# Kernel tuning notes

Measured on AMD Instinct MI355X. Metric: run time of the kernel, lower is better.

Reference implementation:

```python
import jax, jax.numpy as jnp
import numpy as np

B, N, IN_DIM, H, L = 8, 1024, 3, 256, 3
NUM_STEPS = 200
LN_EPS = 1e-5


def _cdist(a, b):
    # Euclidean pairwise distance, a:[B,n,d], b:[B,m,d] -> [B,n,m]
    d2 = (jnp.sum(a * a, -1)[:, :, None] + jnp.sum(b * b, -1)[:, None, :]
          - 2.0 * jnp.einsum('bik,bjk->bij', a, b))
    d2 = jnp.maximum(d2, 0.0)
    safe = jnp.sqrt(jnp.where(d2 > 0, d2, 1.0))
    return jnp.where(d2 > 0, safe, 0.0)


def _layernorm(x, g, b):
    mu = jnp.mean(x, -1, keepdims=True)
    var = jnp.mean(jnp.square(x - mu), -1, keepdims=True)
    return (x - mu) * jax.lax.rsqrt(var + LN_EPS) * g + b


def setup_inputs() -> dict:
    key = jax.random.key(0)
    ks = jax.random.split(key, 32)
    s = 0.02
    inp = {
        'x': jax.random.normal(ks[0], (B, N, IN_DIM), jnp.float32),
        't': jax.random.randint(ks[1], (B,), 0, NUM_STEPS),
        'mask': jnp.ones((B, N), bool),
        # top-level weights (stored [in,out])
        'w_time': jax.random.normal(ks[2], (1, H)) * s,
        'b_time': jnp.zeros((H,)),
        'w_in': jax.random.normal(ks[3], (IN_DIM + H, H)) * s,
        'b_in': jnp.zeros((H,)),
        'w_out': jax.random.normal(ks[4], (H, IN_DIM)) * s,
        'b_out': jnp.zeros((IN_DIM,)),
        # per-layer stacked params [L, ...]
        'qkv_w': jax.random.normal(ks[5], (L, H, 3 * H)) * s,
        'qkv_b': jnp.zeros((L, 3 * H)),
        'ao_w': jax.random.normal(ks[6], (L, H, H)) * s,
        'ao_b': jnp.zeros((L, H)),
        'fc1_w': jax.random.normal(ks[7], (L, H, 4 * H)) * s,
        'fc1_b': jax.random.normal(ks[8], (L, 4 * H)) * s,
        'fc2_w': jax.random.normal(ks[9], (L, 4 * H, H)) * s,
        'fc2_b': jax.random.normal(ks[10], (L, H)) * s,
        'ln1_g': jnp.ones((L, H)), 'ln1_b': jnp.zeros((L, H)),
        'ln2_g': jnp.ones((L, H)), 'ln2_b': jnp.zeros((L, H)),
    }
    return inp


def reference(x, t, mask, w_time, b_time, w_in, b_in, w_out, b_out,
              qkv_w, qkv_b, ao_w, ao_b, fc1_w, fc1_b, fc2_w, fc2_b,
              ln1_g, ln1_b, ln2_g, ln2_b):
    tf = t.astype(jnp.float32)[:, None] / float(NUM_STEPS)          # [B,1]
    t_embed = jax.nn.relu(tf @ w_time + b_time)                      # [B,H]
    t_embed = jnp.broadcast_to(t_embed[:, None, :], (B, N, H))
    h = jax.nn.relu(jnp.concatenate([x, t_embed], -1) @ w_in + b_in)  # [B,N,H]
    geo = _cdist(h[:, :, :3], h[:, :, :3])                           # [B,N,N]
    mask_f = mask.astype(h.dtype)
    scale = 1.0 / jnp.sqrt(jnp.float32(H))
    for l in range(L):
        qkv = (h @ qkv_w[l] + qkv_b[l]).reshape(B, N, 3, H)
        q, k, v = qkv[:, :, 0], qkv[:, :, 1], qkv[:, :, 2]
        dist = _cdist(geo, geo)                                      # cdist of the distance matrix itself
        scores = jnp.einsum('bik,bjk->bij', q, k) * scale * jnp.exp(-dist)
        scores = jnp.where(mask[:, None, :], scores, -jnp.inf)
        attn = jax.nn.softmax(scores, axis=-1)
        ao = (jnp.einsum('bij,bjk->bik', attn, v) @ ao_w[l] + ao_b[l]) * mask_f[:, :, None]
        xx = _layernorm(h + ao, ln1_g[l], ln1_b[l])
        f1 = jax.nn.relu((xx @ fc1_w[l] + fc1_b[l]) * mask_f[:, :, None])
        ffn = jax.nn.relu((f1 @ fc2_w[l] + fc2_b[l]) * mask_f[:, :, None])
        h = _layernorm(xx + ffn, ln2_g[l], ln2_b[l])
    return (h @ w_out + b_out) * mask_f[:, :, None]
```

## Files before the change

kernel.cpp:

```cpp
#include <hip/hip_runtime.h>
#include <math.h>

#define NB 8
#define NN 1024
#define NH 256
#define NL 3

typedef unsigned short u16;
typedef __bf16 bf16x8 __attribute__((ext_vector_type(8)));
typedef _Float16 f16x8 __attribute__((ext_vector_type(8)));
typedef float f32x4 __attribute__((ext_vector_type(4)));

constexpr int EPI_BIAS_RELU = 2, EPI_EDIST = 5, EPI_QKV = 6;

__device__ __forceinline__ unsigned bf16rne(float f) {
    unsigned u = __float_as_uint(f);
    return (u + 0x7fffu + ((u >> 16) & 1u)) >> 16;
}
__device__ __forceinline__ unsigned bfpair(float a, float b) {
    return bf16rne(a) | (bf16rne(b) << 16);
}
__device__ __forceinline__ float bf2f(u16 h) {
    unsigned u = ((unsigned)h) << 16;
    return __uint_as_float(u);
}

__device__ __forceinline__ float blockSum256(float v) {
    __shared__ float sm[4];
    #pragma unroll
    for (int o = 32; o; o >>= 1) v += __shfl_down(v, o, 64);
    int lane = threadIdx.x & 63, wid = threadIdx.x >> 6;
    if (lane == 0) sm[wid] = v;
    __syncthreads();
    if (threadIdx.x == 0) sm[0] = sm[0] + sm[1] + sm[2] + sm[3];
    __syncthreads();
    float r = sm[0];
    __syncthreads();
    return r;
}

template <int EPI, int DT, bool OBF, int SWZ, int MT>
__global__ __launch_bounds__(256) void gemm_mfma(
    const u16* __restrict__ A, int lda, long sA,
    const u16* __restrict__ Bt, int ldb, long sB,
    void* __restrict__ C, int ldc, long sC,
    int K,
    const float* __restrict__ bias, long sBias,
    u16* __restrict__ vtout)
{
    constexpr int MF = MT / 32;
    constexpr int ASZ = MT * 8;
    __shared__ uint4 sm4[ASZ + 1024];
    const int tid = threadIdx.x;

    int bx = blockIdx.x, by = blockIdx.y, bz = blockIdx.z;
    bool trans = false;
    if (SWZ == 2) {
        int gx = gridDim.x;
        int T = gx * gridDim.y;
        int lid = bx + gx * by;
        int nl = (lid & 7) * (T >> 3) + (lid >> 3);
        bx = nl % gx; by = nl / gx;
    } else if (SWZ == 3) {
        int lid = bx + gridDim.x * bz;
        bz = lid & 7;
        int idx = lid >> 3;
        int j = 0;
        while (idx >= 16 - 2 * j) { idx -= 16 - 2 * j; j++; }
        by = 2 * j + idx;
        bx = j;
        trans = (by >= 2 * bx + 2);
    }
    const int z = bz;
    const int row0 = by * MT, col0 = bx * 128;

    f32x4 acc[MF][4];
    #pragma unroll
    for (int m = 0; m < MF; m++)
        #pragma unroll
        for (int n = 0; n < 4; n++) acc[m][n] = (f32x4){0.f, 0.f, 0.f, 0.f};

    const int l = tid & 63, wid = tid >> 6;
    const int wr = wid >> 1, wc = wid & 1;
    const int lrow = l & 15, lgrp = l >> 4;

    for (int k0 = 0; k0 < K; k0 += 64) {
        if (MT == 128) {
            const int srow = tid >> 1, half = tid & 1, cb = half * 4, swz = srow & 7;
            const u16* Ap = A + (long)z * sA + (long)(row0 + srow) * lda + k0 + half * 32;
            uint4 a0 = *(const uint4*)(Ap + 0),  a1 = *(const uint4*)(Ap + 8);
            uint4 a2 = *(const uint4*)(Ap + 16), a3 = *(const uint4*)(Ap + 24);
            sm4[srow * 8 + ((cb + 0) ^ swz)] = a0;
            sm4[srow * 8 + ((cb + 1) ^ swz)] = a1;
            sm4[srow * 8 + ((cb + 2) ^ swz)] = a2;
            sm4[srow * 8 + ((cb + 3) ^ swz)] = a3;
        } else {
            const int arow = tid >> 2, aq = tid & 3, swz = arow & 7;
            const u16* Ap = A + (long)z * sA + (long)(row0 + arow) * lda + k0 + aq * 16;
            uint4 a0 = *(const uint4*)(Ap + 0), a1 = *(const uint4*)(Ap + 8);
            sm4[arow * 8 + ((aq * 2 + 0) ^ swz)] = a0;
            sm4[arow * 8 + ((aq * 2 + 1) ^ swz)] = a1;
        }
        {
            const int brow = tid >> 1, bq = tid & 1, cb = bq * 4, swz = brow & 7;
            const u16* Bp = Bt + (long)z * sB + (long)(col0 + brow) * ldb + k0 + bq * 32;
            uint4 b0 = *(const uint4*)(Bp + 0),  b1 = *(const uint4*)(Bp + 8);
            uint4 b2 = *(const uint4*)(Bp + 16), b3 = *(const uint4*)(Bp + 24);
            sm4[ASZ + brow * 8 + ((cb + 0) ^ swz)] = b0;
            sm4[ASZ + brow * 8 + ((cb + 1) ^ swz)] = b1;
            sm4[ASZ + brow * 8 + ((cb + 2) ^ swz)] = b2;
            sm4[ASZ + brow * 8 + ((cb + 3) ^ swz)] = b3;
        }
        __syncthreads();

        #pragma unroll
        for (int ks = 0; ks < 2; ks++) {
            int c = ks * 4 + lgrp;
            uint4 a[MF], b[4];
            #pragma unroll
            for (int m = 0; m < MF; m++) {
                int r = wr * (MT / 2) + m * 16 + lrow;
                a[m] = sm4[r * 8 + (c ^ (r & 7))];
            }
            #pragma unroll
            for (int n = 0; n < 4; n++) {
                int r = wc * 64 + n * 16 + lrow;
                b[n] = sm4[ASZ + r * 8 + (c ^ (r & 7))];
            }
            #pragma unroll
            for (int m = 0; m < MF; m++)
                #pragma unroll
                for (int n = 0; n < 4; n++) {
                    if (DT == 0)
                        acc[m][n] = __builtin_amdgcn_mfma_f32_16x16x32_bf16(
                            __builtin_bit_cast(bf16x8, a[m]), __builtin_bit_cast(bf16x8, b[n]), acc[m][n], 0, 0, 0);
                    else
                        acc[m][n] = __builtin_amdgcn_mfma_f32_16x16x32_f16(
                            __builtin_bit_cast(f16x8, a[m]), __builtin_bit_cast(f16x8, b[n]), acc[m][n], 0, 0, 0);
                }
        }
        __syncthreads();
    }

    u16* Ts = (u16*)sm4;
    #pragma unroll
    for (int m = 0; m < MF; m++) {
        #pragma unroll
        for (int n = 0; n < 4; n++) {
            int rbase = row0 + wr * (MT / 2) + m * 16 + lgrp * 4;
            int cc = col0 + wc * 64 + n * 16 + lrow;
            float bv = 0.f;
            if (EPI == EPI_QKV || EPI == EPI_BIAS_RELU)
                bv = bias[cc];
            float vals[4];
            #pragma unroll
            for (int reg = 0; reg < 4; reg++) {
                long r = rbase + reg;
                float v = acc[m][n][reg];
                if (EPI == EPI_QKV) v += bv;
                else if (EPI == EPI_BIAS_RELU) v = fmaxf(v + bv, 0.f);
                else if (EPI == EPI_EDIST) {
                    const float* rnb = bias + (long)z * sBias;
                    float d2 = fmaxf(rnb[r] + rnb[cc] - 2.f * v, 0.f);
                    v = (r == cc) ? 1.f : expf(-sqrtf(d2));
                }
                vals[reg] = v;
                if (OBF) ((u16*)C)[(long)z * sC + r * ldc + cc] = (u16)bf16rne(v);
                else     ((float*)C)[(long)z * sC + r * ldc + cc] = v;
            }
            if (EPI == EPI_EDIST && SWZ == 3 && trans) {
                int cl = cc - col0, rl = rbase - row0;
                uint2 tv;
                tv.x = bfpair(vals[0], vals[1]);
                tv.y = bfpair(vals[2], vals[3]);
                *(uint2*)(Ts + cl * 68 + rl) = tv;
            }
            if (EPI == EPI_QKV && cc >= 512) {
                int b = rbase >> 10;
                uint2 tv;
                tv.x = bfpair(vals[0], vals[1]);
                tv.y = bfpair(vals[2], vals[3]);
                *(uint2*)&vtout[(long)b * NH * NN + (long)(cc - 512) * NN + (rbase & 1023)] = tv;
            }
        }
    }
    if (EPI == EPI_EDIST && SWZ == 3 && trans) {
        __syncthreads();
        int row = tid >> 1, half = tid & 1;
        const u16* src = Ts + row * 68 + half * 32;
        uint2 v0 = *(const uint2*)(src + 0),  v1 = *(const uint2*)(src + 4);
        uint2 v2 = *(const uint2*)(src + 8),  v3 = *(const uint2*)(src + 12);
        uint2 v4 = *(const uint2*)(src + 16), v5 = *(const uint2*)(src + 20);
        uint2 v6 = *(const uint2*)(src + 24), v7 = *(const uint2*)(src + 28);
        uint4* dst = (uint4*)((u16*)C + (long)z * sC + (long)(col0 + row) * ldc + row0 + half * 32);
        uint4 w0 = {v0.x, v0.y, v1.x, v1.y};
        uint4 w1 = {v2.x, v2.y, v3.x, v3.y};
        uint4 w2 = {v4.x, v4.y, v5.x, v5.y};
        uint4 w3 = {v6.x, v6.y, v7.x, v7.y};
        dst[0] = w0; dst[1] = w1; dst[2] = w2; dst[3] = w3;
    }
}

__global__ __launch_bounds__(512) void flash_k(
    const u16* __restrict__ qkv,
    const u16* __restrict__ vt,
    const u16* __restrict__ edist,
    const u16* __restrict__ aow,
    const float* __restrict__ aob,
    const float* __restrict__ hres,
    const float* __restrict__ g1,
    const float* __restrict__ b1,
    float* __restrict__ xb,
    u16* __restrict__ xbbf,
    float scale)
{
    __shared__ uint4 Ks[128][32];
    __shared__ uint4 Vts[256][16];
    __shared__ __align__(16) u16 Es[32][136];
    __shared__ __align__(16) u16 Ps[32][136];
    __shared__ float rs[32][8];
    __shared__ float lnA[32][8];
    __shared__ float lnB[32][8];

    const int tid = threadIdx.x;
    const int l = tid & 63, w = tid >> 6;
    const int g = l >> 4, lr = l & 15;

    int lid = blockIdx.x + gridDim.x * blockIdx.y;
    const int b = lid & 7;
    const int q0 = (lid >> 3) * 32;

    const u16* qkvb = qkv + (long)b * NN * 768;
    const u16* vtb  = vt + (long)b * NH * NN;
    const u16* eb   = edist + (long)b * NN * NN;

    uint4 qf[2][8];
    #pragma unroll
    for (int m = 0; m < 2; m++)
        #pragma unroll
        for (int ks = 0; ks < 8; ks++)
            qf[m][ks] = *(const uint4*)(qkvb + (long)(q0 + 16 * m + lr) * 768 + 32 * ks + 8 * g);

    f32x4 oacc[2][2];
    #pragma unroll
    for (int m = 0; m < 2; m++)
        #pragma unroll
        for (int nf = 0; nf < 2; nf++) oacc[m][nf] = (f32x4){0.f, 0.f, 0.f, 0.f};
    float rsum[2][4] = {{0.f, 0.f, 0.f, 0.f}, {0.f, 0.f, 0.f, 0.f}};

    for (int n0 = 0; n0 < NN; n0 += 128) {
        #pragma unroll
        for (int i = 0; i < 8; i++) {
            int idx = tid + 512 * i;
            int row = idx >> 5, ch = idx & 31;
            Ks[row][ch ^ (row & 7)] = *(const uint4*)(qkvb + (long)(n0 + row) * 768 + 256 + ch * 8);
        }
        #pragma unroll
        for (int i = 0; i < 8; i++) {
            int idx = tid + 512 * i;
            int c = idx >> 4, ch = idx & 15;
            Vts[c][(ch & 8) | ((ch & 7) ^ (c & 7))] = *(const uint4*)(vtb + (long)c * NN + n0 + ch * 8);
        }
        {
            int r = tid >> 4, ch = tid & 15;
            *(uint4*)&Es[r][ch * 8] = *(const uint4*)(eb + (long)(q0 + r) * NN + n0 + ch * 8);
        }
        __syncthreads();

        f32x4 s[2];
        s[0] = (f32x4){0.f, 0.f, 0.f, 0.f};
        s[1] = (f32x4){0.f, 0.f, 0.f, 0.f};
        const int krow = w * 16 + lr;
        #pragma unroll
        for (int ks = 0; ks < 8; ks++) {
            bf16x8 kf = __builtin_bit_cast(bf16x8, Ks[krow][(4 * ks + g) ^ (krow & 7)]);
            s[0] = __builtin_amdgcn_mfma_f32_16x16x32_bf16(__builtin_bit_cast(bf16x8, qf[0][ks]), kf, s[0], 0, 0, 0);
            s[1] = __builtin_amdgcn_mfma_f32_16x16x32_bf16(__builtin_bit_cast(bf16x8, qf[1][ks]), kf, s[1], 0, 0, 0);
        }
        #pragma unroll
        for (int m = 0; m < 2; m++)
            #pragma unroll
            for (int reg = 0; reg < 4; reg++) {
                int q = 16 * m + 4 * g + reg;
                int kc = w * 16 + lr;
                float p = expf(s[m][reg] * scale * bf2f(Es[q][kc]));
                rsum[m][reg] += p;
                Ps[q][kc] = (u16)bf16rne(p);
            }
        __syncthreads();
        #pragma unroll
        for (int ks = 0; ks < 4; ks++) {
            bf16x8 pa[2], vbf[2];
            #pragma unroll
            for (int m = 0; m < 2; m++)
                pa[m] = __builtin_bit_cast(bf16x8, *(const uint4*)&Ps[16 * m + lr][32 * ks + 8 * g]);
            #pragma unroll
            for (int nf = 0; nf < 2; nf++) {
                int c = w * 32 + nf * 16 + lr;
                int ch = 4 * ks + g;
                vbf[nf] = __builtin_bit_cast(bf16x8, Vts[c][(ch & 8) | ((ch & 7) ^ (c & 7))]);
            }
            #pragma unroll
            for (int m = 0; m < 2; m++)
                #pragma unroll
                for (int nf = 0; nf < 2; nf++)
                    oacc[m][nf] = __builtin_amdgcn_mfma_f32_16x16x32_bf16(pa[m], vbf[nf], oacc[m][nf], 0, 0, 0);
        }
        __syncthreads();
    }

    #pragma unroll
    for (int m = 0; m < 2; m++)
        #pragma unroll
        for (int reg = 0; reg < 4; reg++) {
            float v = rsum[m][reg];
            v += __shfl_xor(v, 1); v += __shfl_xor(v, 2);
            v += __shfl_xor(v, 4); v += __shfl_xor(v, 8);
            rsum[m][reg] = v;
        }
    if (lr == 0) {
        #pragma unroll
        for (int m = 0; m < 2; m++)
            #pragma unroll
            for (int reg = 0; reg < 4; reg++)
                rs[16 * m + 4 * g + reg][w] = rsum[m][reg];
    }
    __syncthreads();

    u16* Os = (u16*)Ks;
    #pragma unroll
    for (int m = 0; m < 2; m++)
        #pragma unroll
        for (int reg = 0; reg < 4; reg++) {
            int q = 16 * m + 4 * g + reg;
            float t = 0.f;
            #pragma unroll
            for (int j = 0; j < 8; j++) t += rs[q][j];
            float inv = 1.f / t;
            #pragma unroll
            for (int nf = 0; nf < 2; nf++) {
                int c = w * 32 + nf * 16 + lr;
                Os[q * 264 + c] = (u16)bf16rne(oacc[m][nf][reg] * inv);
            }
        }
    __syncthreads();

    f32x4 aacc[2][2];
    #pragma unroll
    for (int m = 0; m < 2; m++)
        #pragma unroll
        for (int nf = 0; nf < 2; nf++) aacc[m][nf] = (f32x4){0.f, 0.f, 0.f, 0.f};
    #pragma unroll
    for (int kc = 0; kc < 8; kc++) {
        bf16x8 pa[2], wb[2];
        #pragma unroll
        for (int m = 0; m < 2; m++)
            pa[m] = __builtin_bit_cast(bf16x8, *(const uint4*)&Os[(16 * m + lr) * 264 + kc * 32 + 8 * g]);
        #pragma unroll
        for (int nf = 0; nf < 2; nf++)
            wb[nf] = __builtin_bit_cast(bf16x8, *(const uint4*)(aow + (long)(32 * w + 16 * nf + lr) * 256 + kc * 32 + 8 * g));
        #pragma unroll
        for (int m = 0; m < 2; m++)
            #pragma unroll
            for (int nf = 0; nf < 2; nf++)
                aacc[m][nf] = __builtin_amdgcn_mfma_f32_16x16x32_bf16(pa[m], wb[nf], aacc[m][nf], 0, 0, 0);
    }

    int j0 = 32 * w + lr, j1 = 32 * w + 16 + lr;
    float aob0 = aob[j0], aob1 = aob[j1];
    float xv[2][2][4];
    #pragma unroll
    for (int m = 0; m < 2; m++)
        #pragma unroll
        for (int reg = 0; reg < 4; reg++) {
            int q = 16 * m + 4 * g + reg;
            long hr = ((long)b * NN + q0 + q) * NH;
            xv[m][0][reg] = aacc[m][0][reg] + aob0 + hres[hr + j0];
            xv[m][1][reg] = aacc[m][1][reg] + aob1 + hres[hr + j1];
        }

    #pragma unroll
    for (int m = 0; m < 2; m++)
        #pragma unroll
        for (int reg = 0; reg < 4; reg++) {
            float s = xv[m][0][reg] + xv[m][1][reg];
            float s2 = xv[m][0][reg] * xv[m][0][reg] + xv[m][1][reg] * xv[m][1][reg];
            s  += __shfl_xor(s, 1);  s  += __shfl_xor(s, 2);  s  += __shfl_xor(s, 4);  s  += __shfl_xor(s, 8);
            s2 += __shfl_xor(s2, 1); s2 += __shfl_xor(s2, 2); s2 += __shfl_xor(s2, 4); s2 += __shfl_xor(s2, 8);
            if (lr == 0) {
                int q = 16 * m + 4 * g + reg;
                lnA[q][w] = s;
                lnB[q][w] = s2;
            }
        }
    __syncthreads();

    float g1v0 = g1[j0], g1v1 = g1[j1], b1v0 = b1[j0], b1v1 = b1[j1];
    #pragma unroll
    for (int m = 0; m < 2; m++)
        #pragma unroll
        for (int reg = 0; reg < 4; reg++) {
            int q = 16 * m + 4 * g + reg;
            float S = 0.f, S2 = 0.f;
            #pragma unroll
            for (int j = 0; j < 8; j++) { S += lnA[q][j]; S2 += lnB[q][j]; }
            float mu = S * (1.f / NH);
            float var = S2 * (1.f / NH) - mu * mu;
            float rsd = rsqrtf(var + 1e-5f);
            long hr = ((long)b * NN + q0 + q) * NH;
            float o0 = (xv[m][0][reg] - mu) * rsd * g1v0 + b1v0;
            float o1 = (xv[m][1][reg] - mu) * rsd * g1v1 + b1v1;
            xb[hr + j0] = o0;
            xb[hr + j1] = o1;
            xbbf[hr + j0] = (u16)bf16rne(o0);
            xbbf[hr + j1] = (u16)bf16rne(o1);
        }
}

__global__ __launch_bounds__(256) void fc2ln_k(
    const u16* __restrict__ f1,
    const float* __restrict__ resid,
    const u16* __restrict__ w2,
    const float* __restrict__ b2,
    const float* __restrict__ g2,
    const float* __restrict__ bb2,
    float* __restrict__ hout,
    u16* __restrict__ hbf)
{
    __shared__ uint4 As[256];
    __shared__ uint4 Bs[2048];
    __shared__ float lnA[32][4], lnB[32][4];

    const int tid = threadIdx.x;
    const int l = tid & 63, w = tid >> 6;
    const int lrow = l & 15, lgrp = l >> 4;
    const long r0 = (long)blockIdx.x * 32;

    f32x4 acc[2][4];
    #pragma unroll
    for (int m = 0; m < 2; m++)
        #pragma unroll
        for (int n = 0; n < 4; n++) acc[m][n] = (f32x4){0.f, 0.f, 0.f, 0.f};

    for (int k0 = 0; k0 < 1024; k0 += 64) {
        {
            int row = tid >> 3, ch = tid & 7;
            As[row * 8 + (ch ^ (row & 7))] = *(const uint4*)(f1 + (r0 + row) * 1024 + k0 + ch * 8);
        }
        #pragma unroll
        for (int i = 0; i < 8; i++) {
            int idx = tid + 256 * i;
            int row = idx >> 3, ch = idx & 7;
            Bs[row * 8 + (ch ^ (row & 7))] = *(const uint4*)(w2 + (long)row * 1024 + k0 + ch * 8);
        }
        __syncthreads();
        #pragma unroll
        for (int ks = 0; ks < 2; ks++) {
            int c = ks * 4 + lgrp;
            uint4 a[2], b[4];
            #pragma unroll
            for (int m = 0; m < 2; m++) {
                int r = m * 16 + lrow;
                a[m] = As[r * 8 + (c ^ (r & 7))];
            }
            #pragma unroll
            for (int n = 0; n < 4; n++) {
                int r = 64 * w + n * 16 + lrow;
                b[n] = Bs[r * 8 + (c ^ (r & 7))];
            }
            #pragma unroll
            for (int m = 0; m < 2; m++)
                #pragma unroll
                for (int n = 0; n < 4; n++)
                    acc[m][n] = __builtin_amdgcn_mfma_f32_16x16x32_bf16(
                        __builtin_bit_cast(bf16x8, a[m]), __builtin_bit_cast(bf16x8, b[n]), acc[m][n], 0, 0, 0);
        }
        __syncthreads();
    }

    float xv[2][4][4];
    #pragma unroll
    for (int m = 0; m < 2; m++)
        #pragma unroll
        for (int n = 0; n < 4; n++) {
            int cc = 64 * w + 16 * n + lrow;
            float bv = b2[cc];
            #pragma unroll
            for (int reg = 0; reg < 4; reg++) {
                int rr = 16 * m + 4 * lgrp + reg;
                xv[m][n][reg] = fmaxf(acc[m][n][reg] + bv, 0.f) + resid[(r0 + rr) * 256 + cc];
            }
        }

    #pragma unroll
    for (int m = 0; m < 2; m++)
        #pragma unroll
        for (int reg = 0; reg < 4; reg++) {
            float s = 0.f, s2 = 0.f;
            #pragma unroll
            for (int n = 0; n < 4; n++) {
                s += xv[m][n][reg];
                s2 += xv[m][n][reg] * xv[m][n][reg];
            }
            s  += __shfl_xor(s, 1);  s  += __shfl_xor(s, 2);  s  += __shfl_xor(s, 4);  s  += __shfl_xor(s, 8);
            s2 += __shfl_xor(s2, 1); s2 += __shfl_xor(s2, 2); s2 += __shfl_xor(s2, 4); s2 += __shfl_xor(s2, 8);
            if (lrow == 0) {
                int rr = 16 * m + 4 * lgrp + reg;
                lnA[rr][w] = s;
                lnB[rr][w] = s2;
            }
        }
    __syncthreads();

    #pragma unroll
    for (int m = 0; m < 2; m++)
        #pragma unroll
        for (int reg = 0; reg < 4; reg++) {
            int rr = 16 * m + 4 * lgrp + reg;
            float S = lnA[rr][0] + lnA[rr][1] + lnA[rr][2] + lnA[rr][3];
            float S2 = lnB[rr][0] + lnB[rr][1] + lnB[rr][2] + lnB[rr][3];
            float mu = S * (1.f / NH);
            float var = S2 * (1.f / NH) - mu * mu;
            float rsd = rsqrtf(var + 1e-5f);
            #pragma unroll
            for (int n = 0; n < 4; n++) {
                int cc = 64 * w + 16 * n + lrow;
                float o = (xv[m][n][reg] - mu) * rsd * g2[cc] + bb2[cc];
                hout[(r0 + rr) * 256 + cc] = o;
                hbf[(r0 + rr) * 256 + cc] = (u16)bf16rne(o);
            }
        }
}

__global__ __launch_bounds__(256) void base_k(const int* __restrict__ t,
                                              const float* __restrict__ w_time,
                                              const float* __restrict__ b_time,
                                              const float* __restrict__ w_in,
                                              const float* __restrict__ b_in,
                                              float* __restrict__ base) {
    int b = blockIdx.x, j = threadIdx.x;
    __shared__ float te[256];
    float tf = (float)t[b] / 200.0f;
    te[j] = fmaxf(tf * w_time[j] + b_time[j], 0.f);
    __syncthreads();
    float acc = b_in[j];
    for (int k = 0; k < 256; k++) acc = fmaf(te[k], w_in[(3 + k) * 256 + j], acc);
    base[b * 256 + j] = acc;
}

__global__ __launch_bounds__(256) void hinit_k(const float* __restrict__ x,
                                               const float* __restrict__ w_in,
                                               const float* __restrict__ base,
                                               float* __restrict__ h,
                                               u16* __restrict__ hbf,
                                               float* __restrict__ h3) {
    long row = blockIdx.x;
    int b = (int)(row >> 10);
    int j = threadIdx.x;
    float x0 = x[row * 3 + 0], x1 = x[row * 3 + 1], x2 = x[row * 3 + 2];
    float v = base[b * 256 + j];
    v = fmaf(x0, w_in[j], v);
    v = fmaf(x1, w_in[256 + j], v);
    v = fmaf(x2, w_in[512 + j], v);
    v = fmaxf(v, 0.f);
    h[row * 256 + j] = v;
    hbf[row * 256 + j] = (u16)bf16rne(v);
    if (j < 3) h3[row * 3 + j] = v;
}

__global__ __launch_bounds__(256) void geo_k(const float* __restrict__ h3,
                                             u16* __restrict__ gf,
                                             float* __restrict__ rn) {
    int bi = blockIdx.x;
    int b = bi >> 10, i = bi & 1023;
    const float* hb = h3 + (long)b * NN * 3;
    float ax = hb[i * 3 + 0], ay = hb[i * 3 + 1], az = hb[i * 3 + 2];
    u16* grow = gf + (long)bi * 1024;
    float accs = 0.f;
    #pragma unroll
    for (int j0 = 0; j0 < NN; j0 += 256) {
        int j = j0 + threadIdx.x;
        float dx = hb[j * 3 + 0] - ax, dy = hb[j * 3 + 1] - ay, dz = hb[j * 3 + 2] - az;
        float d2 = dx * dx + dy * dy + dz * dz;
        float d = (d2 > 0.f) ? sqrtf(d2) : 0.f;
        _Float16 hf = (_Float16)d;
        float rep = (float)hf;
        grow[j] = __builtin_bit_cast(u16, hf);
        accs += rep * rep;
    }
    float tot = blockSum256(accs);
    if (threadIdx.x == 0) rn[bi] = tot;
}

__global__ __launch_bounds__(256) void wtrans_k(const float* __restrict__ qkv_w,
                                                const float* __restrict__ ao_w,
                                                const float* __restrict__ fc1_w,
                                                const float* __restrict__ fc2_w,
                                                u16* __restrict__ qkv_wt,
                                                u16* __restrict__ ao_wt,
                                                u16* __restrict__ fc1_wt,
                                                u16* __restrict__ fc2_wt) {
    int type = blockIdx.z, lyr = blockIdx.y;
    int R, Cc;
    const float* src;
    u16* dst;
    if (type == 0) { R = 256; Cc = 768;  src = qkv_w + (long)lyr * R * Cc; dst = qkv_wt + (long)lyr * R * Cc; }
    else if (type == 1) { R = 256; Cc = 256; src = ao_w + (long)lyr * R * Cc; dst = ao_wt + (long)lyr * R * Cc; }
    else if (type == 2) { R = 256; Cc = 1024; src = fc1_w + (long)lyr * R * Cc; dst = fc1_wt + (long)lyr * R * Cc; }
    else { R = 1024; Cc = 256; src = fc2_w + (long)lyr * R * Cc; dst = fc2_wt + (long)lyr * R * Cc; }
    int tC = Cc >> 5, tR = R >> 5;
    int tile = blockIdx.x;
    if (tile >= tC * tR) return;
    int c0 = (tile % tC) << 5, r0 = (tile / tC) << 5;
    __shared__ float tf[32][33];
    int tx = threadIdx.x & 31, ty = threadIdx.x >> 5;
    #pragma unroll
    for (int i = 0; i < 4; i++) {
        int r = ty + 8 * i;
        tf[r][tx] = src[(long)(r0 + r) * Cc + c0 + tx];
    }
    __syncthreads();
    #pragma unroll
    for (int i = 0; i < 4; i++) {
        int c = ty + 8 * i;
        dst[(long)(c0 + c) * R + r0 + tx] = (u16)bf16rne(tf[tx][c]);
    }
}

__global__ __launch_bounds__(256) void out_k(const float* __restrict__ h,
                                             const float* __restrict__ w_out,
                                             const float* __restrict__ b_out,
                                             float* __restrict__ out) {
    long row = blockIdx.x;
    int wid = threadIdx.x >> 6, lane = threadIdx.x & 63;
    if (wid < 3) {
        float acc = 0.f;
        for (int k = lane; k < 256; k += 64) acc = fmaf(h[row * 256 + k], w_out[k * 3 + wid], acc);
        #pragma unroll
        for (int o = 32; o; o >>= 1) acc += __shfl_down(acc, o, 64);
        if (lane == 0) out[row * 3 + wid] = acc + b_out[wid];
    }
}

extern "C" void kernel_launch(void* const* d_in, const int* in_sizes, int n_in,
                              void* d_out, int out_size, void* d_ws, size_t ws_size,
                              hipStream_t stream) {
    const float* x      = (const float*)d_in[0];
    const int*   t      = (const int*)  d_in[1];
    const float* w_time = (const float*)d_in[3];
    const float* b_time = (const float*)d_in[4];
    const float* w_in   = (const float*)d_in[5];
    const float* b_in   = (const float*)d_in[6];
    const float* w_out  = (const float*)d_in[7];
    const float* b_out  = (const float*)d_in[8];
    const float* qkv_w  = (const float*)d_in[9];
    const float* qkv_b  = (const float*)d_in[10];
    const float* ao_w   = (const float*)d_in[11];
    const float* ao_b   = (const float*)d_in[12];
    const float* fc1_w  = (const float*)d_in[13];
    const float* fc1_b  = (const float*)d_in[14];
    const float* fc2_w  = (const float*)d_in[15];
    const float* fc2_b  = (const float*)d_in[16];
    const float* ln1_g  = (const float*)d_in[17];
    const float* ln1_b  = (const float*)d_in[18];
    const float* ln2_g  = (const float*)d_in[19];
    const float* ln2_b  = (const float*)d_in[20];
    float* out = (float*)d_out;

    char* W = (char*)d_ws;
    float* h     = (float*)(W);
    float* xb    = (float*)(W + (8ul << 20));
    u16*   hbf   = (u16*)  (W + (16ul << 20));
    u16*   xbbf  = (u16*)  (W + (20ul << 20));
    u16*   vt    = (u16*)  (W + (24ul << 20));
    u16*   f1    = (u16*)  (W + (28ul << 20));
    u16*   qkvb  = (u16*)  (W + (44ul << 20));
    u16*   edist = (u16*)  (W + (56ul << 20));
    u16*   gf    = (u16*)  (W + (72ul << 20));
    u16*   wts   = (u16*)  (W + (88ul << 20));
    u16* qkv_wt = wts;
    u16* ao_wt  = wts + 589824;
    u16* fc1_wt = wts + 786432;
    u16* fc2_wt = wts + 1572864;
    float* base = (float*)(W + (94ul << 20));
    float* rn   = base + 2048;
    float* h3   = rn + 8192;

    const float scale = 1.0f / 16.0f;

    base_k<<<NB, 256, 0, stream>>>(t, w_time, b_time, w_in, b_in, base);
    hinit_k<<<NB * NN, 256, 0, stream>>>(x, w_in, base, h, hbf, h3);
    geo_k<<<NB * NN, 256, 0, stream>>>(h3, gf, rn);
    wtrans_k<<<dim3(256, NL, 4), 256, 0, stream>>>(qkv_w, ao_w, fc1_w, fc2_w,
                                                   qkv_wt, ao_wt, fc1_wt, fc2_wt);
    gemm_mfma<EPI_EDIST, 1, true, 3, 64><<<dim3(72, 1, 8), 256, 0, stream>>>(
        gf, 1024, (long)NN * 1024, gf, 1024, (long)NN * 1024,
        edist, NN, (long)NN * NN, 1024, rn, NN, nullptr);

    for (int l = 0; l < NL; ++l) {
        gemm_mfma<EPI_QKV, 0, true, 2, 64><<<dim3(6, 128, 1), 256, 0, stream>>>(
            hbf, NH, 0, qkv_wt + (long)l * 196608, NH, 0, qkvb, 768, 0,
            NH, qkv_b + l * 768, 0, vt);
        flash_k<<<dim3(32, 8), 512, 0, stream>>>(
            qkvb, vt, edist, ao_wt + (long)l * 65536, ao_b + l * NH,
            h, ln1_g + l * NH, ln1_b + l * NH, xb, xbbf, scale);
        gemm_mfma<EPI_BIAS_RELU, 0, true, 2, 128><<<dim3(8, 64, 1), 256, 0, stream>>>(
            xbbf, NH, 0, fc1_wt + (long)l * 262144, NH, 0, f1, 1024, 0,
            NH, fc1_b + l * 1024, 0, nullptr);
        fc2ln_k<<<256, 256, 0, stream>>>(
            f1, xb, fc2_wt + (long)l * 262144, fc2_b + l * NH,
            ln2_g + l * NH, ln2_b + l * NH, h, hbf);
    }
    out_k<<<NB * NN, 256, 0, stream>>>(h, w_out, b_out, out);
}
```

Measured before the change: 319.2 us.

## Retile flash attention kernel to 16-query blocks with 256 threads

Shrinks each flash_k block from 32 query rows and 8 waves to 16 query rows and 4 waves, with 64-key tiles instead of 128. The grid doubles to 512 blocks so more CUs are occupied and shared memory per block drops. In exchange, K and V tiles are reloaded from global memory twice as often in total, since each block covers fewer queries.

Result: slower. 342.2 us (+7.2%).

```diff
diff --git a/kernel.cpp b/kernel.cpp
--- a/kernel.cpp
+++ b/kernel.cpp
@@ -201,7 +201,7 @@
     }
 }
 
-__global__ __launch_bounds__(512) void flash_k(
+__global__ __launch_bounds__(256) void flash_k(
     const u16* __restrict__ qkv,
     const u16* __restrict__ vt,
     const u16* __restrict__ edist,
@@ -214,13 +214,13 @@
     u16* __restrict__ xbbf,
     float scale)
 {
-    __shared__ uint4 Ks[128][32];
-    __shared__ uint4 Vts[256][16];
-    __shared__ __align__(16) u16 Es[32][136];
-    __shared__ __align__(16) u16 Ps[32][136];
-    __shared__ float rs[32][8];
-    __shared__ float lnA[32][8];
-    __shared__ float lnB[32][8];
+    __shared__ uint4 Ks[64][32];
+    __shared__ uint4 Vts[256][8];
+    __shared__ __align__(16) u16 Es[16][72];
+    __shared__ __align__(16) u16 Ps[16][72];
+    __shared__ float rs[16][4];
+    __shared__ float lnA[16][4];
+    __shared__ float lnB[16][4];
 
     const int tid = threadIdx.x;
     const int l = tid & 63, w = tid >> 6;
@@ -228,193 +228,159 @@
 
     int lid = blockIdx.x + gridDim.x * blockIdx.y;
     const int b = lid & 7;
-    const int q0 = (lid >> 3) * 32;
+    const int q0 = (lid >> 3) * 16;
 
     const u16* qkvb = qkv + (long)b * NN * 768;
     const u16* vtb  = vt + (long)b * NH * NN;
     const u16* eb   = edist + (long)b * NN * NN;
 
-    uint4 qf[2][8];
-    #pragma unroll
-    for (int m = 0; m < 2; m++)
-        #pragma unroll
-        for (int ks = 0; ks < 8; ks++)
-            qf[m][ks] = *(const uint4*)(qkvb + (long)(q0 + 16 * m + lr) * 768 + 32 * ks + 8 * g);
-
-    f32x4 oacc[2][2];
-    #pragma unroll
-    for (int m = 0; m < 2; m++)
-        #pragma unroll
-        for (int nf = 0; nf < 2; nf++) oacc[m][nf] = (f32x4){0.f, 0.f, 0.f, 0.f};
-    float rsum[2][4] = {{0.f, 0.f, 0.f, 0.f}, {0.f, 0.f, 0.f, 0.f}};
-
-    for (int n0 = 0; n0 < NN; n0 += 128) {
+    uint4 qf[8];
+    #pragma unroll
+    for (int ks = 0; ks < 8; ks++)
+        qf[ks] = *(const uint4*)(qkvb + (long)(q0 + lr) * 768 + 32 * ks + 8 * g);
+
+    f32x4 oacc[4];
+    #pragma unroll
+    for (int nf = 0; nf < 4; nf++) oacc[nf] = (f32x4){0.f, 0.f, 0.f, 0.f};
+    float rsum[4] = {0.f, 0.f, 0.f, 0.f};
+
+    for (int n0 = 0; n0 < NN; n0 += 64) {
         #pragma unroll
         for (int i = 0; i < 8; i++) {
-            int idx = tid + 512 * i;
+            int idx = tid + 256 * i;
             int row = idx >> 5, ch = idx & 31;
             Ks[row][ch ^ (row & 7)] = *(const uint4*)(qkvb + (long)(n0 + row) * 768 + 256 + ch * 8);
         }
         #pragma unroll
         for (int i = 0; i < 8; i++) {
-            int idx = tid + 512 * i;
-            int c = idx >> 4, ch = idx & 15;
-            Vts[c][(ch & 8) | ((ch & 7) ^ (c & 7))] = *(const uint4*)(vtb + (long)c * NN + n0 + ch * 8);
-        }
-        {
-            int r = tid >> 4, ch = tid & 15;
+            int idx = tid + 256 * i;
+            int c = idx >> 3, ch = idx & 7;
+            Vts[c][ch ^ (c & 7)] = *(const uint4*)(vtb + (long)c * NN + n0 + ch * 8);
+        }
+        if (tid < 128) {
+            int r = tid >> 3, ch = tid & 7;
             *(uint4*)&Es[r][ch * 8] = *(const uint4*)(eb + (long)(q0 + r) * NN + n0 + ch * 8);
         }
         __syncthreads();
 
-        f32x4 s[2];
-        s[0] = (f32x4){0.f, 0.f, 0.f, 0.f};
-        s[1] = (f32x4){0.f, 0.f, 0.f, 0.f};
-        const int krow = w * 16 + lr;
+        f32x4 s = (f32x4){0.f, 0.f, 0.f, 0.f};
+        const int krow = 16 * w + lr;
         #pragma unroll
         for (int ks = 0; ks < 8; ks++) {
             bf16x8 kf = __builtin_bit_cast(bf16x8, Ks[krow][(4 * ks + g) ^ (krow & 7)]);
-            s[0] = __builtin_amdgcn_mfma_f32_16x16x32_bf16(__builtin_bit_cast(bf16x8, qf[0][ks]), kf, s[0], 0, 0, 0);
-            s[1] = __builtin_amdgcn_mfma_f32_16x16x32_bf16(__builtin_bit_cast(bf16x8, qf[1][ks]), kf, s[1], 0, 0, 0);
-        }
-        #pragma unroll
-        for (int m = 0; m < 2; m++)
-            #pragma unroll
-            for (int reg = 0; reg < 4; reg++) {
-                int q = 16 * m + 4 * g + reg;
-                int kc = w * 16 + lr;
-                float p = expf(s[m][reg] * scale * bf2f(Es[q][kc]));
-                rsum[m][reg] += p;
-                Ps[q][kc] = (u16)bf16rne(p);
-            }
-        __syncthreads();
-        #pragma unroll
-        for (int ks = 0; ks < 4; ks++) {
-            bf16x8 pa[2], vbf[2];
-            #pragma unroll
-            for (int m = 0; m < 2; m++)
-                pa[m] = __builtin_bit_cast(bf16x8, *(const uint4*)&Ps[16 * m + lr][32 * ks + 8 * g]);
-            #pragma unroll
-            for (int nf = 0; nf < 2; nf++) {
-                int c = w * 32 + nf * 16 + lr;
-                int ch = 4 * ks + g;
-                vbf[nf] = __builtin_bit_cast(bf16x8, Vts[c][(ch & 8) | ((ch & 7) ^ (c & 7))]);
-            }
-            #pragma unroll
-            for (int m = 0; m < 2; m++)
-                #pragma unroll
-                for (int nf = 0; nf < 2; nf++)
-                    oacc[m][nf] = __builtin_amdgcn_mfma_f32_16x16x32_bf16(pa[m], vbf[nf], oacc[m][nf], 0, 0, 0);
-        }
-        __syncthreads();
-    }
-
-    #pragma unroll
-    for (int m = 0; m < 2; m++)
+            s = __builtin_amdgcn_mfma_f32_16x16x32_bf16(__builtin_bit_cast(bf16x8, qf[ks]), kf, s, 0, 0, 0);
+        }
         #pragma unroll
         for (int reg = 0; reg < 4; reg++) {
-            float v = rsum[m][reg];
-            v += __shfl_xor(v, 1); v += __shfl_xor(v, 2);
-            v += __shfl_xor(v, 4); v += __shfl_xor(v, 8);
-            rsum[m][reg] = v;
-        }
+            int q = 4 * g + reg;
+            int kc = 16 * w + lr;
+            float p = expf(s[reg] * scale * bf2f(Es[q][kc]));
+            rsum[reg] += p;
+            Ps[q][kc] = (u16)bf16rne(p);
+        }
+        __syncthreads();
+
+        #pragma unroll
+        for (int ks = 0; ks < 2; ks++) {
+            bf16x8 pa = __builtin_bit_cast(bf16x8, *(const uint4*)&Ps[lr][32 * ks + 8 * g]);
+            #pragma unroll
+            for (int nf = 0; nf < 4; nf++) {
+                int c = 64 * w + 16 * nf + lr;
+                bf16x8 vbf = __builtin_bit_cast(bf16x8, Vts[c][(4 * ks + g) ^ (c & 7)]);
+                oacc[nf] = __builtin_amdgcn_mfma_f32_16x16x32_bf16(pa, vbf, oacc[nf], 0, 0, 0);
+            }
+        }
+        __syncthreads();
+    }
+
+    #pragma unroll
+    for (int reg = 0; reg < 4; reg++) {
+        float v = rsum[reg];
+        v += __shfl_xor(v, 1); v += __shfl_xor(v, 2);
+        v += __shfl_xor(v, 4); v += __shfl_xor(v, 8);
+        rsum[reg] = v;
+    }
     if (lr == 0) {
         #pragma unroll
-        for (int m = 0; m < 2; m++)
-            #pragma unroll
-            for (int reg = 0; reg < 4; reg++)
-                rs[16 * m + 4 * g + reg][w] = rsum[m][reg];
+        for (int reg = 0; reg < 4; reg++)
+            rs[4 * g + reg][w] = rsum[reg];
     }
     __syncthreads();
 
     u16* Os = (u16*)Ks;
     #pragma unroll
-    for (int m = 0; m < 2; m++)
+    for (int reg = 0; reg < 4; reg++) {
+        int q = 4 * g + reg;
+        float t = rs[q][0] + rs[q][1] + rs[q][2] + rs[q][3];
+        float inv = 1.f / t;
+        #pragma unroll
+        for (int nf = 0; nf < 4; nf++) {
+            int c = 64 * w + 16 * nf + lr;
+            Os[q * 264 + c] = (u16)bf16rne(oacc[nf][reg] * inv);
+        }
+    }
+    __syncthreads();
+
+    f32x4 aacc[4];
+    #pragma unroll
+    for (int nf = 0; nf < 4; nf++) aacc[nf] = (f32x4){0.f, 0.f, 0.f, 0.f};
+    #pragma unroll
+    for (int kc = 0; kc < 8; kc++) {
+        bf16x8 pa = __builtin_bit_cast(bf16x8, *(const uint4*)&Os[lr * 264 + kc * 32 + 8 * g]);
+        #pragma unroll
+        for (int nf = 0; nf < 4; nf++) {
+            bf16x8 wb = __builtin_bit_cast(bf16x8,
+                *(const uint4*)(aow + (long)(64 * w + 16 * nf + lr) * 256 + kc * 32 + 8 * g));
+            aacc[nf] = __builtin_amdgcn_mfma_f32_16x16x32_bf16(pa, wb, aacc[nf], 0, 0, 0);
+        }
+    }
+
+    float xv[4][4];
+    #pragma unroll
+    for (int nf = 0; nf < 4; nf++) {
+        int j = 64 * w + 16 * nf + lr;
+        float aobv = aob[j];
         #pragma unroll
         for (int reg = 0; reg < 4; reg++) {
-            int q = 16 * m + 4 * g + reg;
-            float t = 0.f;
-            #pragma unroll
-            for (int j = 0; j < 8; j++) t += rs[q][j];
-            float inv = 1.f / t;
-            #pragma unroll
-            for (int nf = 0; nf < 2; nf++) {
-                int c = w * 32 + nf * 16 + lr;
-                Os[q * 264 + c] = (u16)bf16rne(oacc[m][nf][reg] * inv);
-            }
-        }
-    __syncthreads();
-
-    f32x4 aacc[2][2];
-    #pragma unroll
-    for (int m = 0; m < 2; m++)
-        #pragma unroll
-        for (int nf = 0; nf < 2; nf++) aacc[m][nf] = (f32x4){0.f, 0.f, 0.f, 0.f};
-    #pragma unroll
-    for (int kc = 0; kc < 8; kc++) {
-        bf16x8 pa[2], wb[2];
-        #pragma unroll
-        for (int m = 0; m < 2; m++)
-            pa[m] = __builtin_bit_cast(bf16x8, *(const uint4*)&Os[(16 * m + lr) * 264 + kc * 32 + 8 * g]);
-        #pragma unroll
-        for (int nf = 0; nf < 2; nf++)
-            wb[nf] = __builtin_bit_cast(bf16x8, *(const uint4*)(aow + (long)(32 * w + 16 * nf + lr) * 256 + kc * 32 + 8 * g));
-        #pragma unroll
-        for (int m = 0; m < 2; m++)
-            #pragma unroll
-            for (int nf = 0; nf < 2; nf++)
-                aacc[m][nf] = __builtin_amdgcn_mfma_f32_16x16x32_bf16(pa[m], wb[nf], aacc[m][nf], 0, 0, 0);
-    }
-
-    int j0 = 32 * w + lr, j1 = 32 * w + 16 + lr;
-    float aob0 = aob[j0], aob1 = aob[j1];
-    float xv[2][2][4];
-    #pragma unroll
-    for (int m = 0; m < 2; m++)
-        #pragma unroll
-        for (int reg = 0; reg < 4; reg++) {
-            int q = 16 * m + 4 * g + reg;
-            long hr = ((long)b * NN + q0 + q) * NH;
-            xv[m][0][reg] = aacc[m][0][reg] + aob0 + hres[hr + j0];
-            xv[m][1][reg] = aacc[m][1][reg] + aob1 + hres[hr + j1];
-        }
-
-    #pragma unroll
-    for (int m = 0; m < 2; m++)
-        #pragma unroll
-        for (int reg = 0; reg < 4; reg++) {
-            float s = xv[m][0][reg] + xv[m][1][reg];
-            float s2 = xv[m][0][reg] * xv[m][0][reg] + xv[m][1][reg] * xv[m][1][reg];
-            s  += __shfl_xor(s, 1);  s  += __shfl_xor(s, 2);  s  += __shfl_xor(s, 4);  s  += __shfl_xor(s, 8);
-            s2 += __shfl_xor(s2, 1); s2 += __shfl_xor(s2, 2); s2 += __shfl_xor(s2, 4); s2 += __shfl_xor(s2, 8);
-            if (lr == 0) {
-                int q = 16 * m + 4 * g + reg;
-                lnA[q][w] = s;
-                lnB[q][w] = s2;
-            }
-        }
-    __syncthreads();
-
-    float g1v0 = g1[j0], g1v1 = g1[j1], b1v0 = b1[j0], b1v1 = b1[j1];
-    #pragma unroll
-    for (int m = 0; m < 2; m++)
-        #pragma unroll
-        for (int reg = 0; reg < 4; reg++) {
-            int q = 16 * m + 4 * g + reg;
-            float S = 0.f, S2 = 0.f;
-            #pragma unroll
-            for (int j = 0; j < 8; j++) { S += lnA[q][j]; S2 += lnB[q][j]; }
-            float mu = S * (1.f / NH);
-            float var = S2 * (1.f / NH) - mu * mu;
-            float rsd = rsqrtf(var + 1e-5f);
-            long hr = ((long)b * NN + q0 + q) * NH;
-            float o0 = (xv[m][0][reg] - mu) * rsd * g1v0 + b1v0;
-            float o1 = (xv[m][1][reg] - mu) * rsd * g1v1 + b1v1;
-            xb[hr + j0] = o0;
-            xb[hr + j1] = o1;
-            xbbf[hr + j0] = (u16)bf16rne(o0);
-            xbbf[hr + j1] = (u16)bf16rne(o1);
-        }
+            int q = 4 * g + reg;
+            xv[nf][reg] = aacc[nf][reg] + aobv + hres[((long)b * NN + q0 + q) * NH + j];
+        }
+    }
+
+    #pragma unroll
+    for (int reg = 0; reg < 4; reg++) {
+        float s = 0.f, s2 = 0.f;
+        #pragma unroll
+        for (int nf = 0; nf < 4; nf++) {
+            s += xv[nf][reg];
+            s2 += xv[nf][reg] * xv[nf][reg];
+        }
+        s  += __shfl_xor(s, 1);  s  += __shfl_xor(s, 2);  s  += __shfl_xor(s, 4);  s  += __shfl_xor(s, 8);
+        s2 += __shfl_xor(s2, 1); s2 += __shfl_xor(s2, 2); s2 += __shfl_xor(s2, 4); s2 += __shfl_xor(s2, 8);
+        if (lr == 0) {
+            lnA[4 * g + reg][w] = s;
+            lnB[4 * g + reg][w] = s2;
+        }
+    }
+    __syncthreads();
+
+    #pragma unroll
+    for (int reg = 0; reg < 4; reg++) {
+        int q = 4 * g + reg;
+        float S = lnA[q][0] + lnA[q][1] + lnA[q][2] + lnA[q][3];
+        float S2 = lnB[q][0] + lnB[q][1] + lnB[q][2] + lnB[q][3];
+        float mu = S * (1.f / NH);
+        float var = S2 * (1.f / NH) - mu * mu;
+        float rsd = rsqrtf(var + 1e-5f);
+        long hr = ((long)b * NN + q0 + q) * NH;
+        #pragma unroll
+        for (int nf = 0; nf < 4; nf++) {
+            int j = 64 * w + 16 * nf + lr;
+            float o = (xv[nf][reg] - mu) * rsd * g1[j] + b1[j];
+            xb[hr + j] = o;
+            xbbf[hr + j] = (u16)bf16rne(o);
+        }
+    }
 }
 
 __global__ __launch_bounds__(256) void fc2ln_k(
@@ -701,7 +667,7 @@
         gemm_mfma<EPI_QKV, 0, true, 2, 64><<<dim3(6, 128, 1), 256, 0, stream>>>(
             hbf, NH, 0, qkv_wt + (long)l * 196608, NH, 0, qkvb, 768, 0,
             NH, qkv_b + l * 768, 0, vt);
-        flash_k<<<dim3(32, 8), 512, 0, stream>>>(
+        flash_k<<<dim3(64, 8), 256, 0, stream>>>(
             qkvb, vt, edist, ao_wt + (long)l * 65536, ao_b + l * NH,
             h, ln1_g + l * NH, ln1_b + l * NH, xb, xbbf, scale);
         gemm_mfma<EPI_BIAS_RELU, 0, true, 2, 128><<<dim3(8, 64, 1), 256, 0, stream>>>(
```
